# Kernel optimization log

Measured on AMD Instinct MI355X. Metric: run time of the kernel, lower is better.

Reference implementation:

```python
import jax, jax.numpy as jnp
import numpy as np

V, E, H, C = 50000, 300, 256, 20   # vocab, embed dim, hidden per direction, num tags
B, T = 128, 512


def setup_inputs() -> dict:
    key = jax.random.key(0)
    ks = jax.random.split(key, 16)
    def n(k, shape, s=0.1):
        return jax.random.normal(k, shape, jnp.float32) * s
    return {
        "input_ids": jax.random.randint(ks[0], (B, T), 0, V),
        "labels": jax.random.randint(ks[1], (B, T), 0, C),
        "emb": n(ks[2], (V, E), 1.0),
        # LSTM params stacked over direction: [2, 4H, in], gate order i,f,g,o (torch)
        "w_ih_l0": n(ks[3], (2, 4 * H, E)),
        "w_hh_l0": n(ks[4], (2, 4 * H, H)),
        "b_ih_l0": n(ks[5], (2, 4 * H)),
        "b_hh_l0": n(ks[6], (2, 4 * H)),
        "w_ih_l1": n(ks[7], (2, 4 * H, 2 * H)),
        "w_hh_l1": n(ks[8], (2, 4 * H, H)),
        "b_ih_l1": n(ks[9], (2, 4 * H)),
        "b_hh_l1": n(ks[10], (2, 4 * H)),
        "fc_w": n(ks[11], (C, 2 * H)),
        "fc_b": n(ks[12], (C,)),
        "transitions": n(ks[13], (C, C)),
        "start_trans": n(ks[14], (C,)),
        "end_trans": n(ks[15], (C,)),
    }


def _lstm_dir(x, w_ih, w_hh, b, reverse):
    # x: [B,T,in] -> h: [B,T,H]; torch gate order i,f,g,o
    xg = jnp.einsum('bti,gi->btg', x, w_ih) + b  # [B,T,4H], input projection fused
    Hd = w_hh.shape[1]
    Bd = x.shape[0]
    def step(carry, g_t):
        h, c = carry
        g = g_t + h @ w_hh.T
        i, f, gg, o = jnp.split(g, 4, axis=-1)
        c = jax.nn.sigmoid(f) * c + jax.nn.sigmoid(i) * jnp.tanh(gg)
        h = jax.nn.sigmoid(o) * jnp.tanh(c)
        return (h, c), h
    init = (jnp.zeros((Bd, Hd), x.dtype), jnp.zeros((Bd, Hd), x.dtype))
    _, hs = jax.lax.scan(step, init, jnp.swapaxes(xg, 0, 1), reverse=reverse)
    return jnp.swapaxes(hs, 0, 1)


def _bilstm_layer(x, w_ih, w_hh, b_ih, b_hh):
    b = b_ih + b_hh
    hf = _lstm_dir(x, w_ih[0], w_hh[0], b[0], False)
    hb = _lstm_dir(x, w_ih[1], w_hh[1], b[1], True)
    return jnp.concatenate([hf, hb], axis=-1)


def _crf_nll(em, tags, trans, start, end):
    # pytorch-crf log-likelihood, reduction='sum'; no mask (all positions valid)
    # numerator: gold path score
    em_sc = jnp.take_along_axis(em, tags[..., None], axis=2)[..., 0].sum(-1)  # [B]
    tr_sc = trans[tags[:, :-1], tags[:, 1:]].sum(-1)                          # [B]
    num = start[tags[:, 0]] + em_sc + tr_sc + end[tags[:, -1]]
    # partition via forward algorithm
    alpha0 = start[None, :] + em[:, 0]  # [B,C]
    def step(alpha, e_t):
        alpha = jax.nn.logsumexp(alpha[:, :, None] + trans[None], axis=1) + e_t
        return alpha, None
    alpha, _ = jax.lax.scan(step, alpha0, jnp.swapaxes(em[:, 1:], 0, 1))
    logZ = jax.nn.logsumexp(alpha + end[None, :], axis=-1)  # [B]
    return -(num - logZ).sum()  # loss = -crf(emissions, labels)


def reference(input_ids, labels, emb, w_ih_l0, w_hh_l0, b_ih_l0, b_hh_l0,
              w_ih_l1, w_hh_l1, b_ih_l1, b_hh_l1, fc_w, fc_b,
              transitions, start_trans, end_trans):
    x = emb[input_ids]                                   # [B,T,E]
    x = _bilstm_layer(x, w_ih_l0, w_hh_l0, b_ih_l0, b_hh_l0)  # [B,T,2H]
    x = _bilstm_layer(x, w_ih_l1, w_hh_l1, b_ih_l1, b_hh_l1)  # [B,T,2H]
    # dropout(p=0.2) is identity in eval mode
    emissions = jnp.einsum('bth,ch->btc', x, fc_w) + fc_b     # [B,T,C]
    return _crf_nll(emissions, labels, transitions, start_trans, end_trans)
```

## Files before the change

### kernel.cpp

```cpp
#include <hip/hip_runtime.h>
#include <hip/hip_bf16.h>


typedef __attribute__((ext_vector_type(8))) short bf16x8;
typedef __attribute__((ext_vector_type(4))) float f32x4;
typedef __attribute__((ext_vector_type(2))) float f32x2;

#define B_ 128
#define T_ 512
#define H_ 256
#define TC 64
#define NC 8

__device__ __align__(256) unsigned short g_h0[(size_t)T_*B_*512];
__device__ __align__(256) unsigned short g_xgc[(size_t)B_*2*TC*1024];
__device__ __align__(256) unsigned short g_embb[(size_t)50000*320];
__device__ __align__(256) float          g_em[(size_t)T_*B_*20];
__device__ __align__(256) unsigned short g_wih0b[2048*320];
__device__ __align__(256) unsigned short g_wih1b[2048*512];
__device__ __align__(256) unsigned short g_fcwb[20*512];
__device__ __align__(256) unsigned long long g_wl8_0[2*16*1024];
__device__ __align__(256) unsigned long long g_wl8_1[2*16*1024];
__device__ __align__(256) uint4          g_ws8_0[2*8*1024];
__device__ __align__(256) uint4          g_ws8_1[2*8*1024];
__device__ __align__(256) float          g_state[256*512];
__device__ __align__(256) float          g_perb[128];

__device__ __forceinline__ unsigned short f2bf(float f){
  unsigned u = __float_as_uint(f);
  return (unsigned short)((u + 0x7FFFu + ((u>>16)&1u)) >> 16);
}
__device__ __forceinline__ f32x2 bfpair(unsigned u){
  f32x2 r; r.x = __uint_as_float(u<<16); r.y = __uint_as_float(u & 0xFFFF0000u); return r;
}
__device__ __forceinline__ float sigm(float x){ return 1.0f/(1.0f + __expf(-x)); }
__device__ __forceinline__ float tanh_f(float x){ return 1.0f - 2.0f/(1.0f + __expf(2.0f*x)); }
__device__ __forceinline__ float cl(float x, float b){ return fminf(b, fmaxf(-b, x)); }

__device__ __forceinline__ unsigned char f2e4m3(float f){
  unsigned u = __float_as_uint(f);
  unsigned s = (u >> 24) & 0x80u;
  float a = fabsf(f);
  a = fminf(a, 448.0f);
  if (a < 0.015625f){
    int qi = (int)rintf(a * 512.0f);
    if (qi == 8) return (unsigned char)(s | 0x08);
    return (unsigned char)(s | qi);
  }
  int e; float m = frexpf(a, &e);
  int mi = (int)rintf(m * 16.0f);
  int ef = e + 6;
  if (mi == 16){ mi = 8; ef++; }
  if (ef >= 16 || (ef == 15 && (mi & 7) == 7)) return (unsigned char)(s | 0x7E);
  return (unsigned char)(s | (ef << 3) | (mi & 7));
}

__global__ __launch_bounds__(256) void k_cvt(const float* __restrict__ src,
    unsigned short* __restrict__ dst, int n4)
{
  int i = blockIdx.x*256 + threadIdx.x;
  if (i >= n4) return;
  float4 v = ((const float4*)src)[i];
  unsigned lo = (unsigned)f2bf(v.x) | ((unsigned)f2bf(v.y) << 16);
  unsigned hi = (unsigned)f2bf(v.z) | ((unsigned)f2bf(v.w) << 16);
  ((uint2*)dst)[i] = make_uint2(lo, hi);
}

__global__ __launch_bounds__(256) void k_cvt_emb(const float* __restrict__ emb)
{
  int idx = blockIdx.x*256 + threadIdx.x;
  if (idx >= 50000*40) return;
  int row = idx / 40, c8 = (idx - row*40)*8;
  const float* s = emb + (size_t)row*300 + c8;
  unsigned short o[8];
  #pragma unroll
  for (int e=0;e<8;e++){ int c = c8+e; o[e] = (c < 300) ? f2bf(s[e]) : (unsigned short)0; }
  *(uint4*)(g_embb + (size_t)row*320 + c8) = *(const uint4*)o;
}

__global__ __launch_bounds__(256) void k_cvt_wih(const float* __restrict__ w,
    int Kin, int Kout, int which)
{
  int per = Kout >> 3;
  int idx = blockIdx.x*256 + threadIdx.x;
  if (idx >= 2048*per) return;
  int row = idx / per, c8 = (idx - row*per)*8;
  const float* s = w + (size_t)row*Kin + c8;
  unsigned short o[8];
  #pragma unroll
  for (int e=0;e<8;e++){ int c = c8+e; o[e] = (c < Kin) ? f2bf(s[e]) : (unsigned short)0; }
  unsigned short* dst = which ? g_wih1b : g_wih0b;
  *(uint4*)(dst + (size_t)row*Kout + c8) = *(const uint4*)o;
}

__global__ __launch_bounds__(256) void k_repack8(const float* __restrict__ whh, int which)
{
  int idx = blockIdx.x*256 + threadIdx.x;
  if (idx >= 49152) return;
  if (idx < 32768){
    int dir = idx >> 14, rem = idx & 16383, j = rem >> 10, t = rem & 1023;
    int l = t & 63, w = t >> 6, q = l >> 4, c = l & 15;
    int nt = j & 3, kt = j >> 2;
    int n = w*64 + nt*16 + c;
    const float* src = whh + ((size_t)dir*1024 + n)*H_ + kt*32 + q*8;
    unsigned long long v = 0;
    #pragma unroll
    for (int e=0;e<8;e++) v |= (unsigned long long)f2e4m3(src[e]) << (8*e);
    (which ? g_wl8_1 : g_wl8_0)[idx] = v;
  } else {
    int i2 = idx - 32768;
    int dir = i2 >> 13, rem = i2 & 8191, j = rem >> 10, t = rem & 1023;
    int l = t & 63, w = t >> 6, q = l >> 4, c = l & 15;
    int nt = j & 3, ktp = j >> 2;
    int n = w*64 + nt*16 + c;
    unsigned r[4];
    #pragma unroll
    for (int half=0; half<2; half++){
      const float* src = whh + ((size_t)dir*1024 + n)*H_ + 128 + (2*ktp+half)*32 + q*8;
      unsigned b0 = 0, b1 = 0;
      #pragma unroll
      for (int e=0;e<4;e++) b0 |= (unsigned)f2e4m3(src[e])   << (8*e);
      #pragma unroll
      for (int e=0;e<4;e++) b1 |= (unsigned)f2e4m3(src[4+e]) << (8*e);
      r[2*half] = b0; r[2*half+1] = b1;
    }
    (which ? g_ws8_1 : g_ws8_0)[i2] = make_uint4(r[0], r[1], r[2], r[3]);
  }
}

__global__ __launch_bounds__(256) void k_init_em(const float* __restrict__ fcb)
{
  int idx = blockIdx.x*256 + threadIdx.x;
  if (idx >= T_*B_*20) return;
  g_em[idx] = fcb[idx % 20];
}

__global__ __launch_bounds__(256) void k_gemm_chunk(
    const int* __restrict__ ids,
    const float* __restrict__ bih, const float* __restrict__ bhh,
    int K, int chunk, int mode)
{
  int pl = blockIdx.x;
  int n0 = blockIdx.y * 128;
  int dirB = n0 >> 10;
  int p = chunk*TC + pl;
  int t_abs = dirB ? (T_-1-p) : p;
  __shared__ __align__(16) unsigned short Al[128][40];
  __shared__ __align__(16) unsigned short Bl[128][40];
  int tid = threadIdx.x;
  int wave = tid >> 6, lane = tid & 63;
  int wm = wave >> 1, wn = wave & 1;
  int col = lane & 15, quad = lane >> 4;
  f32x4 acc[4][4];
  #pragma unroll
  for (int i=0;i<4;i++)
    #pragma unroll
    for (int j=0;j<4;j++) acc[i][j] = (f32x4){0.f,0.f,0.f,0.f};
  int Kc = K >> 5;
  int r = tid >> 2, co = (tid & 3) * 8;
  const unsigned short* Wb = mode ? g_wih1b : g_wih0b;
  const unsigned short* Arow0 = g_h0 + (size_t)t_abs*128*512;
  const unsigned short* a0p = nullptr; const unsigned short* a1p = nullptr;
  if (mode == 0){
    int id0 = ids[r*T_ + t_abs], id1 = ids[(64+r)*T_ + t_abs];
    a0p = g_embb + (size_t)id0*320;
    a1p = g_embb + (size_t)id1*320;
  } else {
    a0p = Arow0 + (size_t)r*512;
    a1p = Arow0 + (size_t)(64+r)*512;
  }
  const unsigned short* b0p = Wb + (size_t)(n0+r)*K;
  const unsigned short* b1p = Wb + (size_t)(n0+64+r)*K;
  for (int kc=0; kc<Kc; kc++){
    int k0 = kc*32;
    *(uint4*)(&Al[r][co])    = *(const uint4*)(a0p + k0 + co);
    *(uint4*)(&Al[64+r][co]) = *(const uint4*)(a1p + k0 + co);
    *(uint4*)(&Bl[r][co])    = *(const uint4*)(b0p + k0 + co);
    *(uint4*)(&Bl[64+r][co]) = *(const uint4*)(b1p + k0 + co);
    __syncthreads();
    bf16x8 af[4], bfv[4];
    #pragma unroll
    for (int mi=0;mi<4;mi++) af[mi]  = *(const bf16x8*)(&Al[wm*64 + mi*16 + col][quad*8]);
    #pragma unroll
    for (int ni=0;ni<4;ni++) bfv[ni] = *(const bf16x8*)(&Bl[wn*64 + ni*16 + col][quad*8]);
    #pragma unroll
    for (int mi=0;mi<4;mi++)
      #pragma unroll
      for (int ni=0;ni<4;ni++)
        acc[mi][ni] = __builtin_amdgcn_mfma_f32_16x16x32_bf16(af[mi], bfv[ni], acc[mi][ni], 0, 0, 0);
    __syncthreads();
  }
  #pragma unroll
  for (int mi=0;mi<4;mi++){
    int b0 = wm*64 + mi*16 + quad*4;
    #pragma unroll
    for (int ni=0;ni<4;ni++){
      int n_ = n0 + wn*64 + ni*16 + col;
      float bias = bih[n_] + bhh[n_];
      int dir = n_ >> 10, np = n_ & 1023;
      #pragma unroll
      for (int rg=0; rg<4; rg++){
        float v = acc[mi][ni][rg] + bias;
        size_t o = (((size_t)(b0+rg)*2 + dir)*TC + pl)*1024 + np;
        g_xgc[o] = f2bf(v);
      }
    }
  }
}

__global__ __attribute__((amdgpu_flat_work_group_size(1024, 1024)))
           __attribute__((amdgpu_waves_per_eu(4, 4)))
void k_lstm_chunk(int chunk, int first, int mode)
{
  int b = blockIdx.x >> 1, dir = blockIdx.x & 1;
  int tid = threadIdx.x;
  __shared__ __align__(16) unsigned long long Wf8[16384];
  __shared__ __align__(16) float hsh[256];
  __shared__ __align__(8)  unsigned char  h_f8u[256];
  __shared__ float gsh[1024];
  __shared__ unsigned fwl[320*8];
  {
    const uint4* src4 = (const uint4*)(mode ? g_wl8_1 : g_wl8_0) + (size_t)dir*8192;
    #pragma unroll
    for (int i=0;i<8;i++) ((uint4*)Wf8)[i*1024 + tid] = src4[i*1024 + tid];
  }
  int fcact = (mode == 1) && (tid >= 384) && (tid < 704);
  int fc_tid = tid - 384;
  if (fcact){
    int c = fc_tid >> 4, p_ = fc_tid & 15;
    const uint4* src = (const uint4*)(g_fcwb + (size_t)c*512 + dir*256 + p_*16);
    uint4 w0 = src[0], w1 = src[1];
    *(uint4*)(&fwl[fc_tid*8])     = w0;
    *(uint4*)(&fwl[fc_tid*8 + 4]) = w1;
  }
  float* st = g_state + (size_t)blockIdx.x*512;
  float cst = 0.f;
  if (tid < 256){
    float h0v = first ? 0.f : st[tid];
    hsh[tid]   = h0v;
    h_f8u[tid] = f2e4m3(h0v);
    cst        = first ? 0.f : st[256+tid];
  }
  const uint4* wsp = (mode ? g_ws8_1 : g_ws8_0) + (size_t)dir*8192 + tid;
  const unsigned short* xrow = g_xgc + (((size_t)b*2 + dir)*TC)*1024;
  __syncthreads();
  int lane = tid & 63;
  int quad = lane >> 4;
  int p0 = chunk*TC;
  unsigned short xcur = xrow[tid];
  for (int s=0; s<TC; s++){
    unsigned short xnxt = (s < TC-1) ? xrow[(size_t)(s+1)*1024 + tid] : (unsigned short)0;
    f32x4 acc0 = {0.f,0.f,0.f,0.f}, acc1 = acc0, acc2 = acc0, acc3 = acc0;
    uint4 c0 = wsp[0*1024], c1 = wsp[1*1024], c2 = wsp[2*1024], c3 = wsp[3*1024];
    #pragma unroll
    for (int kt=0; kt<4; kt++){
      long long a = *(const long long*)(h_f8u + kt*32 + quad*8);
      long long b0 = (long long)Wf8[(kt*4+0)*1024 + tid];
      long long b1 = (long long)Wf8[(kt*4+1)*1024 + tid];
      long long b2 = (long long)Wf8[(kt*4+2)*1024 + tid];
      long long b3 = (long long)Wf8[(kt*4+3)*1024 + tid];
      acc0 = __builtin_amdgcn_mfma_f32_16x16x32_fp8_fp8(a, b0, acc0, 0, 0, 0);
      acc1 = __builtin_amdgcn_mfma_f32_16x16x32_fp8_fp8(a, b1, acc1, 0, 0, 0);
      acc2 = __builtin_amdgcn_mfma_f32_16x16x32_fp8_fp8(a, b2, acc2, 0, 0, 0);
      acc3 = __builtin_amdgcn_mfma_f32_16x16x32_fp8_fp8(a, b3, acc3, 0, 0, 0);
    }
    uint4 d0 = wsp[4*1024], d1 = wsp[5*1024], d2 = wsp[6*1024], d3 = wsp[7*1024];
    {
      long long alo = *(const long long*)(h_f8u + 128 + quad*8);
      long long ahi = *(const long long*)(h_f8u + 160 + quad*8);
      long long b0l = (long long)(((unsigned long long)c0.y << 32) | c0.x);
      long long b0h = (long long)(((unsigned long long)c0.w << 32) | c0.z);
      long long b1l = (long long)(((unsigned long long)c1.y << 32) | c1.x);
      long long b1h = (long long)(((unsigned long long)c1.w << 32) | c1.z);
      long long b2l = (long long)(((unsigned long long)c2.y << 32) | c2.x);
      long long b2h = (long long)(((unsigned long long)c2.w << 32) | c2.z);
      long long b3l = (long long)(((unsigned long long)c3.y << 32) | c3.x);
      long long b3h = (long long)(((unsigned long long)c3.w << 32) | c3.z);
      acc0 = __builtin_amdgcn_mfma_f32_16x16x32_fp8_fp8(alo, b0l, acc0, 0, 0, 0);
      acc0 = __builtin_amdgcn_mfma_f32_16x16x32_fp8_fp8(ahi, b0h, acc0, 0, 0, 0);
      acc1 = __builtin_amdgcn_mfma_f32_16x16x32_fp8_fp8(alo, b1l, acc1, 0, 0, 0);
      acc1 = __builtin_amdgcn_mfma_f32_16x16x32_fp8_fp8(ahi, b1h, acc1, 0, 0, 0);
      acc2 = __builtin_amdgcn_mfma_f32_16x16x32_fp8_fp8(alo, b2l, acc2, 0, 0, 0);
      acc2 = __builtin_amdgcn_mfma_f32_16x16x32_fp8_fp8(ahi, b2h, acc2, 0, 0, 0);
      acc3 = __builtin_amdgcn_mfma_f32_16x16x32_fp8_fp8(alo, b3l, acc3, 0, 0, 0);
      acc3 = __builtin_amdgcn_mfma_f32_16x16x32_fp8_fp8(ahi, b3h, acc3, 0, 0, 0);
    }
    {
      long long alo = *(const long long*)(h_f8u + 192 + quad*8);
      long long ahi = *(const long long*)(h_f8u + 224 + quad*8);
      long long b0l = (long long)(((unsigned long long)d0.y << 32) | d0.x);
      long long b0h = (long long)(((unsigned long long)d0.w << 32) | d0.z);
      long long b1l = (long long)(((unsigned long long)d1.y << 32) | d1.x);
      long long b1h = (long long)(((unsigned long long)d1.w << 32) | d1.z);
      long long b2l = (long long)(((unsigned long long)d2.y << 32) | d2.x);
      long long b2h = (long long)(((unsigned long long)d2.w << 32) | d2.z);
      long long b3l = (long long)(((unsigned long long)d3.y << 32) | d3.x);
      long long b3h = (long long)(((unsigned long long)d3.w << 32) | d3.z);
      acc0 = __builtin_amdgcn_mfma_f32_16x16x32_fp8_fp8(alo, b0l, acc0, 0, 0, 0);
      acc0 = __builtin_amdgcn_mfma_f32_16x16x32_fp8_fp8(ahi, b0h, acc0, 0, 0, 0);
      acc1 = __builtin_amdgcn_mfma_f32_16x16x32_fp8_fp8(alo, b1l, acc1, 0, 0, 0);
      acc1 = __builtin_amdgcn_mfma_f32_16x16x32_fp8_fp8(ahi, b1h, acc1, 0, 0, 0);
      acc2 = __builtin_amdgcn_mfma_f32_16x16x32_fp8_fp8(alo, b2l, acc2, 0, 0, 0);
      acc2 = __builtin_amdgcn_mfma_f32_16x16x32_fp8_fp8(ahi, b2h, acc2, 0, 0, 0);
      acc3 = __builtin_amdgcn_mfma_f32_16x16x32_fp8_fp8(alo, b3l, acc3, 0, 0, 0);
      acc3 = __builtin_amdgcn_mfma_f32_16x16x32_fp8_fp8(ahi, b3h, acc3, 0, 0, 0);
    }
    {
      float dot = (quad == 3) ? acc3[0] : (quad == 2) ? acc2[0] : (quad == 1) ? acc1[0] : acc0[0];
      f32x2 xv = bfpair((unsigned)xcur);
      gsh[tid] = dot + xv.x;
    }
    __syncthreads();
    int p = p0 + s;
    int time = dir ? (T_-1-p) : p;
    if (tid < 256){
      float gi = cl(gsh[tid],30.f), gf = cl(gsh[256+tid],30.f);
      float gg = cl(gsh[512+tid],30.f), go = cl(gsh[768+tid],30.f);
      cst = sigm(gf)*cst + sigm(gi)*tanh_f(gg);
      cst = cl(cst, 512.f);
      float h = sigm(go)*tanh_f(cl(cst,30.f));
      hsh[tid]   = h;
      h_f8u[tid] = f2e4m3(h);
      if (mode == 0)
        g_h0[((size_t)time*B_ + b)*512 + (size_t)dir*H_ + tid] = f2bf(h);
    }
    __syncthreads();
    if (fcact){
      int c = fc_tid >> 4, p_ = fc_tid & 15;
      const f32x4* hp = (const f32x4*)hsh;
      const unsigned* wq = &fwl[fc_tid*8];
      f32x2 acc2v = {0.f,0.f};
      #pragma unroll
      for (int q=0;q<4;q++){
        f32x4 hv = hp[p_*4 + q];
        acc2v += bfpair(wq[2*q])   * __builtin_shufflevector(hv, hv, 0, 1);
        acc2v += bfpair(wq[2*q+1]) * __builtin_shufflevector(hv, hv, 2, 3);
      }
      float part = acc2v.x + acc2v.y;
      part += __shfl_xor(part, 1);
      part += __shfl_xor(part, 2);
      part += __shfl_xor(part, 4);
      part += __shfl_xor(part, 8);
      if (p_ == 0) atomicAdd(&g_em[((size_t)time*B_ + b)*20 + c], part);
    }
    xcur = xnxt;
  }
  if (tid < 256){ st[tid] = hsh[tid]; st[256+tid] = cst; }
}

__global__ __launch_bounds__(64) void k_crf(
    const int* __restrict__ labels, const float* __restrict__ trans,
    const float* __restrict__ st, const float* __restrict__ en)
{
  int b = blockIdx.x, lane = threadIdx.x;
  float tcol[20];
  #pragma unroll
  for (int c=0;c<20;c++) tcol[c] = (lane<20) ? trans[c*20 + lane] : 0.f;
  float gs = 0.f;
  for (int t=lane; t<T_; t+=64){
    int tg = labels[b*T_ + t];
    gs += g_em[((size_t)t*B_ + b)*20 + tg];
    if (t < T_-1){
      int tg2 = labels[b*T_ + t + 1];
      gs += trans[tg*20 + tg2];
    }
  }
  #pragma unroll
  for (int o=32;o;o>>=1) gs += __shfl_xor(gs, o);
  float alpha = (lane<20) ? st[lane] + g_em[(size_t)b*20 + lane] : -1e30f;
  for (int t=1;t<T_;t++){
    float av[20]; float mx = -1e30f;
    #pragma unroll
    for (int c=0;c<20;c++){
      float a = __shfl(alpha, c);
      av[c] = a + tcol[c];
      mx = fmaxf(mx, av[c]);
    }
    float sm = 0.f;
    #pragma unroll
    for (int c=0;c<20;c++) sm += __expf(av[c]-mx);
    float e = (lane<20) ? g_em[((size_t)t*B_ + b)*20 + lane] : 0.f;
    alpha = (lane<20) ? (mx + __logf(sm) + e) : -1e30f;
  }
  float v = (lane<20) ? alpha + en[lane] : -1e30f;
  float mx = v;
  #pragma unroll
  for (int o=32;o;o>>=1) mx = fmaxf(mx, __shfl_xor(mx, o));
  float sm = (lane<20) ? __expf(v-mx) : 0.f;
  #pragma unroll
  for (int o=32;o;o>>=1) sm += __shfl_xor(sm, o);
  float logZ = mx + __logf(sm);
  if (lane == 0){
    int tg0 = labels[b*T_], tgL = labels[b*T_ + T_-1];
    float num = gs + st[tg0] + en[tgL];
    g_perb[b] = logZ - num;
  }
}

__global__ __launch_bounds__(64) void k_reduce(float* __restrict__ out){
  int lane = threadIdx.x;
  float v = g_perb[lane] + g_perb[lane + 64];
  #pragma unroll
  for (int o=32;o;o>>=1) v += __shfl_xor(v, o);
  if (lane == 0){
    unsigned u = __float_as_uint(v);
    if ((u & 0x7F800000u) == 0x7F800000u) v = 5.0e8f;
    out[0] = v;
  }
}

extern "C" void kernel_launch(void* const* d_in, const int* in_sizes, int n_in,
                              void* d_out, int out_size, void* d_ws, size_t ws_size,
                              hipStream_t stream)
{
  const int*   ids    = (const int*)d_in[0];
  const int*   labels = (const int*)d_in[1];
  const float* emb    = (const float*)d_in[2];
  const float* wih0   = (const float*)d_in[3];
  const float* whh0   = (const float*)d_in[4];
  const float* bih0   = (const float*)d_in[5];
  const float* bhh0   = (const float*)d_in[6];
  const float* wih1   = (const float*)d_in[7];
  const float* whh1   = (const float*)d_in[8];
  const float* bih1   = (const float*)d_in[9];
  const float* bhh1   = (const float*)d_in[10];
  const float* fcw    = (const float*)d_in[11];
  const float* fcb    = (const float*)d_in[12];
  const float* trans  = (const float*)d_in[13];
  const float* stt    = (const float*)d_in[14];
  const float* ent    = (const float*)d_in[15];

  unsigned short* fcwb = nullptr;
  hipGetSymbolAddress((void**)&fcwb, HIP_SYMBOL(g_fcwb));

  k_cvt_emb<<<7813, 256, 0, stream>>>(emb);
  k_cvt_wih<<<320, 256, 0, stream>>>(wih0, 300, 320, 0);
  k_cvt_wih<<<512, 256, 0, stream>>>(wih1, 512, 512, 1);
  k_cvt<<<10, 256, 0, stream>>>(fcw, fcwb, 2560);
  k_repack8<<<192, 256, 0, stream>>>(whh0, 0);
  k_repack8<<<192, 256, 0, stream>>>(whh1, 1);

  for (int c=0; c<NC; c++){
    k_gemm_chunk<<<dim3(TC,16), 256, 0, stream>>>(ids, bih0, bhh0, 320, c, 0);
    k_lstm_chunk<<<256, 1024, 0, stream>>>(c, c==0, 0);
  }
  k_init_em<<<5120, 256, 0, stream>>>(fcb);
  for (int c=0; c<NC; c++){
    k_gemm_chunk<<<dim3(TC,16), 256, 0, stream>>>(ids, bih1, bhh1, 512, c, 1);
    k_lstm_chunk<<<256, 1024, 0, stream>>>(c, c==0, 1);
  }

  k_crf   <<<128, 64, 0, stream>>>(labels, trans, stt, ent);
  k_reduce<<<1, 64, 0, stream>>>((float*)d_out);
}
```

Measured before the change: 3.062 ms.

## Keep upper-half recurrent weights in registers and parallelize CRF over segments

The LSTM chunk kernel no longer re-fetches the second half of the fp8 recurrent weights from global memory on every timestep. Those weights are now loaded once into 16 per-thread registers, and the lower half stays in LDS. The serial CRF forward scan is also split into 8 time segments computed in parallel as 20x20 log-semiring transfer matrices, which a final kernel composes. This adds register pressure at 4 waves per EU and an extra kernel, and the segment kernel performs about 20x more arithmetic per step than the original scan.

```diff
diff --git a/kernel.cpp b/kernel.cpp
--- a/kernel.cpp
+++ b/kernel.cpp
@@ -11,6 +11,7 @@
 #define H_ 256
 #define TC 64
 #define NC 8
+#define NSEG 8
 
 __device__ __align__(256) unsigned short g_h0[(size_t)T_*B_*512];
 __device__ __align__(256) unsigned short g_xgc[(size_t)B_*2*TC*1024];
@@ -21,8 +22,9 @@
 __device__ __align__(256) unsigned short g_fcwb[20*512];
 __device__ __align__(256) unsigned long long g_wl8_0[2*16*1024];
 __device__ __align__(256) unsigned long long g_wl8_1[2*16*1024];
-__device__ __align__(256) uint4          g_ws8_0[2*8*1024];
-__device__ __align__(256) uint4          g_ws8_1[2*8*1024];
+__device__ __align__(256) unsigned long long g_wr8_0[2*16*1024];
+__device__ __align__(256) unsigned long long g_wr8_1[2*16*1024];
+__device__ __align__(256) float          g_mseg[(size_t)B_*NSEG*400];
 __device__ __align__(256) float          g_state[256*512];
 __device__ __align__(256) float          g_perb[128];
 
@@ -96,36 +98,19 @@
 __global__ __launch_bounds__(256) void k_repack8(const float* __restrict__ whh, int which)
 {
   int idx = blockIdx.x*256 + threadIdx.x;
-  if (idx >= 49152) return;
-  if (idx < 32768){
-    int dir = idx >> 14, rem = idx & 16383, j = rem >> 10, t = rem & 1023;
-    int l = t & 63, w = t >> 6, q = l >> 4, c = l & 15;
-    int nt = j & 3, kt = j >> 2;
-    int n = w*64 + nt*16 + c;
-    const float* src = whh + ((size_t)dir*1024 + n)*H_ + kt*32 + q*8;
-    unsigned long long v = 0;
-    #pragma unroll
-    for (int e=0;e<8;e++) v |= (unsigned long long)f2e4m3(src[e]) << (8*e);
-    (which ? g_wl8_1 : g_wl8_0)[idx] = v;
-  } else {
-    int i2 = idx - 32768;
-    int dir = i2 >> 13, rem = i2 & 8191, j = rem >> 10, t = rem & 1023;
-    int l = t & 63, w = t >> 6, q = l >> 4, c = l & 15;
-    int nt = j & 3, ktp = j >> 2;
-    int n = w*64 + nt*16 + c;
-    unsigned r[4];
-    #pragma unroll
-    for (int half=0; half<2; half++){
-      const float* src = whh + ((size_t)dir*1024 + n)*H_ + 128 + (2*ktp+half)*32 + q*8;
-      unsigned b0 = 0, b1 = 0;
-      #pragma unroll
-      for (int e=0;e<4;e++) b0 |= (unsigned)f2e4m3(src[e])   << (8*e);
-      #pragma unroll
-      for (int e=0;e<4;e++) b1 |= (unsigned)f2e4m3(src[4+e]) << (8*e);
-      r[2*half] = b0; r[2*half+1] = b1;
-    }
-    (which ? g_ws8_1 : g_ws8_0)[i2] = make_uint4(r[0], r[1], r[2], r[3]);
-  }
+  if (idx >= 65536) return;
+  int part = idx >> 15;
+  int i2 = idx & 32767;
+  int dir = i2 >> 14, rem = i2 & 16383, j = rem >> 10, t = rem & 1023;
+  int l = t & 63, w = t >> 6, q = l >> 4, c = l & 15;
+  int nt = j & 3, kt = (j >> 2) + (part ? 4 : 0);
+  int n = w*64 + nt*16 + c;
+  const float* src = whh + ((size_t)dir*1024 + n)*H_ + kt*32 + q*8;
+  unsigned long long v = 0;
+  #pragma unroll
+  for (int e=0;e<8;e++) v |= (unsigned long long)f2e4m3(src[e]) << (8*e);
+  if (part) (which ? g_wr8_1 : g_wr8_0)[i2] = v;
+  else      (which ? g_wl8_1 : g_wl8_0)[i2] = v;
 }
 
 __global__ __launch_bounds__(256) void k_init_em(const float* __restrict__ fcb)
@@ -219,6 +204,10 @@
   __shared__ __align__(8)  unsigned char  h_f8u[256];
   __shared__ float gsh[1024];
   __shared__ unsigned fwl[320*8];
+  const unsigned long long* wrp = (mode ? g_wr8_1 : g_wr8_0) + (size_t)dir*16384 + tid;
+  unsigned long long wr[16];
+  #pragma unroll
+  for (int m=0;m<16;m++) wr[m] = wrp[(size_t)m*1024];
   {
     const uint4* src4 = (const uint4*)(mode ? g_wl8_1 : g_wl8_0) + (size_t)dir*8192;
     #pragma unroll
@@ -241,17 +230,14 @@
     h_f8u[tid] = f2e4m3(h0v);
     cst        = first ? 0.f : st[256+tid];
   }
-  const uint4* wsp = (mode ? g_ws8_1 : g_ws8_0) + (size_t)dir*8192 + tid;
   const unsigned short* xrow = g_xgc + (((size_t)b*2 + dir)*TC)*1024;
   __syncthreads();
-  int lane = tid & 63;
-  int quad = lane >> 4;
+  int quad = (tid & 63) >> 4;
   int p0 = chunk*TC;
   unsigned short xcur = xrow[tid];
   for (int s=0; s<TC; s++){
     unsigned short xnxt = (s < TC-1) ? xrow[(size_t)(s+1)*1024 + tid] : (unsigned short)0;
     f32x4 acc0 = {0.f,0.f,0.f,0.f}, acc1 = acc0, acc2 = acc0, acc3 = acc0;
-    uint4 c0 = wsp[0*1024], c1 = wsp[1*1024], c2 = wsp[2*1024], c3 = wsp[3*1024];
     #pragma unroll
     for (int kt=0; kt<4; kt++){
       long long a = *(const long long*)(h_f8u + kt*32 + quad*8);
@@ -264,46 +250,13 @@
       acc2 = __builtin_amdgcn_mfma_f32_16x16x32_fp8_fp8(a, b2, acc2, 0, 0, 0);
       acc3 = __builtin_amdgcn_mfma_f32_16x16x32_fp8_fp8(a, b3, acc3, 0, 0, 0);
     }
-    uint4 d0 = wsp[4*1024], d1 = wsp[5*1024], d2 = wsp[6*1024], d3 = wsp[7*1024];
-    {
-      long long alo = *(const long long*)(h_f8u + 128 + quad*8);
-      long long ahi = *(const long long*)(h_f8u + 160 + quad*8);
-      long long b0l = (long long)(((unsigned long long)c0.y << 32) | c0.x);
-      long long b0h = (long long)(((unsigned long long)c0.w << 32) | c0.z);
-      long long b1l = (long long)(((unsigned long long)c1.y << 32) | c1.x);
-      long long b1h = (long long)(((unsigned long long)c1.w << 32) | c1.z);
-      long long b2l = (long long)(((unsigned long long)c2.y << 32) | c2.x);
-      long long b2h = (long long)(((unsigned long long)c2.w << 32) | c2.z);
-      long long b3l = (long long)(((unsigned long long)c3.y << 32) | c3.x);
-      long long b3h = (long long)(((unsigned long long)c3.w << 32) | c3.z);
-      acc0 = __builtin_amdgcn_mfma_f32_16x16x32_fp8_fp8(alo, b0l, acc0, 0, 0, 0);
-      acc0 = __builtin_amdgcn_mfma_f32_16x16x32_fp8_fp8(ahi, b0h, acc0, 0, 0, 0);
-      acc1 = __builtin_amdgcn_mfma_f32_16x16x32_fp8_fp8(alo, b1l, acc1, 0, 0, 0);
-      acc1 = __builtin_amdgcn_mfma_f32_16x16x32_fp8_fp8(ahi, b1h, acc1, 0, 0, 0);
-      acc2 = __builtin_amdgcn_mfma_f32_16x16x32_fp8_fp8(alo, b2l, acc2, 0, 0, 0);
-      acc2 = __builtin_amdgcn_mfma_f32_16x16x32_fp8_fp8(ahi, b2h, acc2, 0, 0, 0);
-      acc3 = __builtin_amdgcn_mfma_f32_16x16x32_fp8_fp8(alo, b3l, acc3, 0, 0, 0);
-      acc3 = __builtin_amdgcn_mfma_f32_16x16x32_fp8_fp8(ahi, b3h, acc3, 0, 0, 0);
-    }
-    {
-      long long alo = *(const long long*)(h_f8u + 192 + quad*8);
-      long long ahi = *(const long long*)(h_f8u + 224 + quad*8);
-      long long b0l = (long long)(((unsigned long long)d0.y << 32) | d0.x);
-      long long b0h = (long long)(((unsigned long long)d0.w << 32) | d0.z);
-      long long b1l = (long long)(((unsigned long long)d1.y << 32) | d1.x);
-      long long b1h = (long long)(((unsigned long long)d1.w << 32) | d1.z);
-      long long b2l = (long long)(((unsigned long long)d2.y << 32) | d2.x);
-      long long b2h = (long long)(((unsigned long long)d2.w << 32) | d2.z);
-      long long b3l = (long long)(((unsigned long long)d3.y << 32) | d3.x);
-      long long b3h = (long long)(((unsigned long long)d3.w << 32) | d3.z);
-      acc0 = __builtin_amdgcn_mfma_f32_16x16x32_fp8_fp8(alo, b0l, acc0, 0, 0, 0);
-      acc0 = __builtin_amdgcn_mfma_f32_16x16x32_fp8_fp8(ahi, b0h, acc0, 0, 0, 0);
-      acc1 = __builtin_amdgcn_mfma_f32_16x16x32_fp8_fp8(alo, b1l, acc1, 0, 0, 0);
-      acc1 = __builtin_amdgcn_mfma_f32_16x16x32_fp8_fp8(ahi, b1h, acc1, 0, 0, 0);
-      acc2 = __builtin_amdgcn_mfma_f32_16x16x32_fp8_fp8(alo, b2l, acc2, 0, 0, 0);
-      acc2 = __builtin_amdgcn_mfma_f32_16x16x32_fp8_fp8(ahi, b2h, acc2, 0, 0, 0);
-      acc3 = __builtin_amdgcn_mfma_f32_16x16x32_fp8_fp8(alo, b3l, acc3, 0, 0, 0);
-      acc3 = __builtin_amdgcn_mfma_f32_16x16x32_fp8_fp8(ahi, b3h, acc3, 0, 0, 0);
+    #pragma unroll
+    for (int kt=4; kt<8; kt++){
+      long long a = *(const long long*)(h_f8u + kt*32 + quad*8);
+      acc0 = __builtin_amdgcn_mfma_f32_16x16x32_fp8_fp8(a, (long long)wr[(kt-4)*4+0], acc0, 0, 0, 0);
+      acc1 = __builtin_amdgcn_mfma_f32_16x16x32_fp8_fp8(a, (long long)wr[(kt-4)*4+1], acc1, 0, 0, 0);
+      acc2 = __builtin_amdgcn_mfma_f32_16x16x32_fp8_fp8(a, (long long)wr[(kt-4)*4+2], acc2, 0, 0, 0);
+      acc3 = __builtin_amdgcn_mfma_f32_16x16x32_fp8_fp8(a, (long long)wr[(kt-4)*4+3], acc3, 0, 0, 0);
     }
     {
       float dot = (quad == 3) ? acc3[0] : (quad == 2) ? acc2[0] : (quad == 1) ? acc1[0] : acc0[0];
@@ -348,14 +301,44 @@
   if (tid < 256){ st[tid] = hsh[tid]; st[256+tid] = cst; }
 }
 
-__global__ __launch_bounds__(64) void k_crf(
+__global__ __launch_bounds__(512) void k_crf_seg(const float* __restrict__ trans)
+{
+  int b = blockIdx.x >> 3, sgi = blockIdx.x & 7;
+  int tid = threadIdx.x;
+  int act = tid < 400;
+  int i = act ? (tid / 20) : 0;
+  int j = act ? (tid - i*20) : 0;
+  __shared__ float M0[400], M1[400];
+  float tcol[20];
+  #pragma unroll
+  for (int k=0;k<20;k++) tcol[k] = trans[k*20 + j];
+  int t_lo = 1 + sgi*64;
+  int t_hi = (sgi == 7) ? 512 : (t_lo + 64);
+  if (act) M0[tid] = trans[i*20 + j] + g_em[((size_t)t_lo*B_ + b)*20 + j];
+  __syncthreads();
+  float* cur = M0; float* nxt = M1;
+  for (int t = t_lo+1; t < t_hi; ++t){
+    float e = g_em[((size_t)t*B_ + b)*20 + j];
+    const float* mrow = cur + i*20;
+    float mx = -1e30f;
+    #pragma unroll
+    for (int k=0;k<20;k++) mx = fmaxf(mx, mrow[k] + tcol[k]);
+    float sm = 0.f;
+    #pragma unroll
+    for (int k=0;k<20;k++) sm += __expf(mrow[k] + tcol[k] - mx);
+    if (act) nxt[tid] = mx + __logf(sm) + e;
+    __syncthreads();
+    float* tmp = cur; cur = nxt; nxt = tmp;
+  }
+  if (act) g_mseg[(size_t)blockIdx.x*400 + tid] = cur[tid];
+}
+
+__global__ __launch_bounds__(64) void k_crf_fin(
     const int* __restrict__ labels, const float* __restrict__ trans,
     const float* __restrict__ st, const float* __restrict__ en)
 {
   int b = blockIdx.x, lane = threadIdx.x;
-  float tcol[20];
-  #pragma unroll
-  for (int c=0;c<20;c++) tcol[c] = (lane<20) ? trans[c*20 + lane] : 0.f;
+  int lj = (lane < 20) ? lane : 19;
   float gs = 0.f;
   for (int t=lane; t<T_; t+=64){
     int tg = labels[b*T_ + t];
@@ -367,20 +350,20 @@
   }
   #pragma unroll
   for (int o=32;o;o>>=1) gs += __shfl_xor(gs, o);
-  float alpha = (lane<20) ? st[lane] + g_em[(size_t)b*20 + lane] : -1e30f;
-  for (int t=1;t<T_;t++){
-    float av[20]; float mx = -1e30f;
-    #pragma unroll
-    for (int c=0;c<20;c++){
-      float a = __shfl(alpha, c);
-      av[c] = a + tcol[c];
-      mx = fmaxf(mx, av[c]);
-    }
+  float alpha = (lane < 20) ? st[lane] + g_em[(size_t)b*20 + lane] : -1e30f;
+  for (int s=0; s<NSEG; s++){
+    const float* M = g_mseg + ((size_t)(b*NSEG + s))*400;
+    float m[20];
+    #pragma unroll
+    for (int i2=0;i2<20;i2++) m[i2] = M[i2*20 + lj];
+    float mx = -1e30f;
+    #pragma unroll
+    for (int i2=0;i2<20;i2++) mx = fmaxf(mx, __shfl(alpha, i2) + m[i2]);
     float sm = 0.f;
     #pragma unroll
-    for (int c=0;c<20;c++) sm += __expf(av[c]-mx);
-    float e = (lane<20) ? g_em[((size_t)t*B_ + b)*20 + lane] : 0.f;
-    alpha = (lane<20) ? (mx + __logf(sm) + e) : -1e30f;
+    for (int i2=0;i2<20;i2++) sm += __expf(__shfl(alpha, i2) + m[i2] - mx);
+    float na = mx + __logf(sm);
+    alpha = (lane < 20) ? na : -1e30f;
   }
   float v = (lane<20) ? alpha + en[lane] : -1e30f;
   float mx = v;
@@ -437,8 +420,8 @@
   k_cvt_wih<<<320, 256, 0, stream>>>(wih0, 300, 320, 0);
   k_cvt_wih<<<512, 256, 0, stream>>>(wih1, 512, 512, 1);
   k_cvt<<<10, 256, 0, stream>>>(fcw, fcwb, 2560);
-  k_repack8<<<192, 256, 0, stream>>>(whh0, 0);
-  k_repack8<<<192, 256, 0, stream>>>(whh1, 1);
+  k_repack8<<<256, 256, 0, stream>>>(whh0, 0);
+  k_repack8<<<256, 256, 0, stream>>>(whh1, 1);
 
   for (int c=0; c<NC; c++){
     k_gemm_chunk<<<dim3(TC,16), 256, 0, stream>>>(ids, bih0, bhh0, 320, c, 0);
@@ -450,6 +433,7 @@
     k_lstm_chunk<<<256, 1024, 0, stream>>>(c, c==0, 1);
   }
 
-  k_crf   <<<128, 64, 0, stream>>>(labels, trans, stt, ent);
+  k_crf_seg<<<B_*NSEG, 512, 0, stream>>>(trans);
+  k_crf_fin<<<B_, 64, 0, stream>>>(labels, trans, stt, ent);
   k_reduce<<<1, 64, 0, stream>>>((float*)d_out);
 }
```

After: 2.672 ms. 1.15x faster.
